# Optimization experiments

Measured on AMD Instinct MI355X. Metric: run time of the kernel, lower is better.

The kernel has to match this reference:

```python
import jax, jax.numpy as jnp
import numpy as np

N_NODES = 100000
N_EDGES = 3200000
F_IN, HIDDEN, N_CLASSES = 512, 256, 40


def setup_inputs() -> dict:
    key = jax.random.key(0)
    ks = jax.random.split(key, 8)
    x = jax.random.normal(ks[0], (N_NODES, F_IN), dtype=jnp.float32)
    edge_row = jax.random.randint(ks[1], (N_EDGES,), 0, N_NODES, dtype=jnp.int64)
    edge_col = jax.random.randint(ks[2], (N_EDGES,), 0, N_NODES, dtype=jnp.int64)
    edge_val = jax.random.uniform(ks[3], (N_EDGES,), dtype=jnp.float32)
    # Xavier-uniform-ish weights
    lim1 = float(np.sqrt(6.0 / (F_IN + HIDDEN)))
    lim2 = float(np.sqrt(6.0 / (HIDDEN + N_CLASSES)))
    W1 = jax.random.uniform(ks[4], (F_IN, HIDDEN), minval=-lim1, maxval=lim1, dtype=jnp.float32)
    b1 = jnp.zeros((HIDDEN,), dtype=jnp.float32)
    W2 = jax.random.uniform(ks[5], (HIDDEN, N_CLASSES), minval=-lim2, maxval=lim2, dtype=jnp.float32)
    b2 = jnp.zeros((N_CLASSES,), dtype=jnp.float32)
    return {"x": x, "edge_row": edge_row, "edge_col": edge_col, "edge_val": edge_val,
            "W1": W1, "b1": b1, "W2": W2, "b2": b2}


def _spmm(edge_row, edge_col, edge_val, h):
    # out[r] = sum_e val[e] * h[col[e]] for edges with row[e]==r  (a @ h)
    msg = edge_val[:, None] * h[edge_col]            # [E, F] gather + scale
    return jax.ops.segment_sum(msg, edge_row, num_segments=N_NODES)


def reference(x, edge_row, edge_col, edge_val, W1, b1, W2, b2):
    # Layer 1: dense mm -> spmm -> bias -> relu (dropout in eval mode = identity)
    h = _spmm(edge_row, edge_col, edge_val, x @ W1) + b1
    h = jax.nn.relu(h)
    # Layer 2: dense mm -> spmm -> bias
    logits = _spmm(edge_row, edge_col, edge_val, h @ W2) + b2
    return jax.nn.log_softmax(logits, axis=1)
```

## Files before the change

kernel.cpp:

```cpp
#include <hip/hip_runtime.h>
#include <math.h>

#define NN  100000
#define NE  3200000
#define FIN 512
#define HID 256
#define NC  40

#define NBUK 391
#define SPB  9472
#define BIN_BLOCKS 512
#define CHUNK ((NE + BIN_BLOCKS - 1) / BIN_BLOCKS)
#define COLMASK 0x1FFFF

typedef __attribute__((ext_vector_type(8))) short short8;
typedef __attribute__((ext_vector_type(4))) float f32x4;

__device__ inline float bf2f(unsigned short u) {
    unsigned int x = ((unsigned int)u) << 16;
    return __builtin_bit_cast(float, x);
}
__device__ inline unsigned short f2bfu(float f) {
    unsigned int x = __builtin_bit_cast(unsigned int, f);
    unsigned int r = (x + 0x7fffu + ((x >> 16) & 1u)) >> 16;
    return (unsigned short)r;
}
__device__ inline signed char q8(float v, float s) {
    int q = (int)rintf(v * s);
    q = max(-127, min(127, q));
    return (signed char)q;
}
__device__ inline unsigned cvtpk_bf16(float lo, float hi) {
    unsigned r;
    asm("v_cvt_pk_bf16_f32 %0, %1, %2" : "=v"(r) : "v"(lo), "v"(hi));
    return r;
}

__global__ __launch_bounds__(256) void k_bin(const int* __restrict__ er, const int* __restrict__ ec,
                                             const float* __restrict__ ev, int* __restrict__ bcnt,
                                             int2* __restrict__ spack) {
    __shared__ int hist[NBUK];
    __shared__ int base[NBUK];
    __shared__ int lcur[NBUK];
    for (int i = threadIdx.x; i < NBUK; i += 256) { hist[i] = 0; lcur[i] = 0; }
    __syncthreads();
    int start = blockIdx.x * CHUNK;
    int end = min(start + CHUNK, NE);
    for (int e = start + threadIdx.x; e < end; e += 256)
        atomicAdd(&hist[er[e] >> 8], 1);
    __syncthreads();
    for (int i = threadIdx.x; i < NBUK; i += 256) {
        int h = hist[i];
        base[i] = h ? atomicAdd(&bcnt[i], h) : 0;
    }
    __syncthreads();
    for (int e = start + threadIdx.x; e < end; e += 256) {
        int r = er[e];
        int b = r >> 8;
        int ofs = atomicAdd(&lcur[b], 1);
        int2 p;
        p.x = ((r & 255) << 17) | ec[e];
        p.y = __builtin_bit_cast(int, ev[e]);
        spack[(size_t)b * SPB + base[b] + ofs] = p;
    }
}

__global__ __launch_bounds__(256) void k_finecsr(const int2* __restrict__ spack, const int* __restrict__ bcnt,
                                                 int2* __restrict__ cpack,
                                                 int* __restrict__ row_beg, int* __restrict__ row_cnt) {
    __shared__ int cnt[256];
    __shared__ int sm[256];
    __shared__ int cur[256];
    int tid = threadIdx.x;
    int buk = blockIdx.x;
    size_t bb = (size_t)buk * SPB;
    int n = min(bcnt[buk], SPB);
    cnt[tid] = 0;
    __syncthreads();
    for (int i = tid; i < n; i += 256) {
        int lr = ((unsigned)spack[bb + i].x) >> 17;
        atomicAdd(&cnt[lr], 1);
    }
    __syncthreads();
    int v = cnt[tid];
    sm[tid] = v;
    __syncthreads();
    for (int off = 1; off < 256; off <<= 1) {
        int t = (tid >= off) ? sm[tid - off] : 0;
        __syncthreads();
        sm[tid] += t;
        __syncthreads();
    }
    int ex = sm[tid] - v;
    cur[tid] = ex;
    int grow = buk * 256 + tid;
    if (grow < NN) {
        row_beg[grow] = (int)bb + ex;
        row_cnt[grow] = v;
    }
    __syncthreads();
    for (int i = tid; i < n; i += 256) {
        int2 p = spack[bb + i];
        int lr = ((unsigned)p.x) >> 17;
        int pos = atomicAdd(&cur[lr], 1);
        int2 q;
        q.x = p.x & COLMASK;
        q.y = p.y;
        cpack[bb + pos] = q;
    }
}

__global__ __launch_bounds__(256) void k_w1t(const float* __restrict__ W1, unsigned short* __restrict__ W1T) {
    int b = blockIdx.x;
    int n = threadIdx.x;
    unsigned short tmp[16];
#pragma unroll
    for (int kk = 0; kk < 16; kk++)
        tmp[kk] = f2bfu(W1[(size_t)(b * 16 + kk) * HID + n]);
    unsigned short* dst = W1T + (size_t)n * FIN + b * 16;
    *(short8*)dst = *(short8*)tmp;
    *(short8*)(dst + 8) = *(short8*)(tmp + 8);
}

__global__ __launch_bounds__(256) void k_w2t(const float* __restrict__ W2, unsigned short* __restrict__ W2T) {
    int n = blockIdx.x;
    int k = threadIdx.x;
    float v = (n < NC) ? W2[(size_t)k * NC + n] : 0.f;
    W2T[(size_t)n * HID + k] = f2bfu(v);
}

__global__ __launch_bounds__(256) void k_gemm1(const float* __restrict__ x, const unsigned short* __restrict__ W1T,
                                               signed char* __restrict__ h1) {
    __shared__ unsigned short As[2][128][40];
    __shared__ unsigned short Bs[2][128][40];
    const int tid = threadIdx.x;
    const int row0 = (blockIdx.x >> 1) * 128;
    const int col0 = (blockIdx.x & 1) * 128;
    const int lane = tid & 63;
    const int w = tid >> 6;
    const int wr = (w >> 1) * 64;
    const int wc = (w & 1) * 64;
    const int m16 = lane & 15;
    const int quad = lane >> 4;

    const int srow = tid >> 1;
    const int skoff = (tid & 1) * 16;
    int gar = row0 + srow;
    if (gar >= NN) gar = NN - 1;
    const float* ax = x + (size_t)gar * FIN + skoff;
    const unsigned short* bw = W1T + (size_t)(col0 + srow) * FIN + skoff;

    f32x4 acc[4][4];
#pragma unroll
    for (int i = 0; i < 4; i++)
#pragma unroll
        for (int j = 0; j < 4; j++) acc[i][j] = (f32x4){0.f, 0.f, 0.f, 0.f};

    float4 va[4];
    uint4 vb0, vb1;

#define G1_LOAD(tt)                                                        \
    {                                                                      \
        const float* ap = ax + (tt) * 32;                                  \
        va[0] = *(const float4*)(ap);                                      \
        va[1] = *(const float4*)(ap + 4);                                  \
        va[2] = *(const float4*)(ap + 8);                                  \
        va[3] = *(const float4*)(ap + 12);                                 \
        const unsigned short* bp = bw + (tt) * 32;                         \
        vb0 = *(const uint4*)(bp);                                         \
        vb1 = *(const uint4*)(bp + 8);                                     \
    }

#define G1_STORE(bf)                                                       \
    {                                                                      \
        uint4 pa0, pa1;                                                    \
        pa0.x = cvtpk_bf16(va[0].x, va[0].y);                              \
        pa0.y = cvtpk_bf16(va[0].z, va[0].w);                              \
        pa0.z = cvtpk_bf16(va[1].x, va[1].y);                              \
        pa0.w = cvtpk_bf16(va[1].z, va[1].w);                              \
        pa1.x = cvtpk_bf16(va[2].x, va[2].y);                              \
        pa1.y = cvtpk_bf16(va[2].z, va[2].w);                              \
        pa1.z = cvtpk_bf16(va[3].x, va[3].y);                              \
        pa1.w = cvtpk_bf16(va[3].z, va[3].w);                              \
        *(uint4*)(&As[bf][srow][skoff]) = pa0;                             \
        *(uint4*)(&As[bf][srow][skoff + 8]) = pa1;                         \
        *(uint4*)(&Bs[bf][srow][skoff]) = vb0;                             \
        *(uint4*)(&Bs[bf][srow][skoff + 8]) = vb1;                         \
    }

    G1_LOAD(0)
    G1_STORE(0)
    G1_LOAD(1)
    __syncthreads();

    for (int t = 0; t < 16; ++t) {
        const int buf = t & 1;
        short8 af[4], bfr[4];
#pragma unroll
        for (int i = 0; i < 4; i++) af[i] = *(const short8*)(&As[buf][wr + i * 16 + m16][quad * 8]);
#pragma unroll
        for (int j = 0; j < 4; j++) bfr[j] = *(const short8*)(&Bs[buf][wc + j * 16 + m16][quad * 8]);
        if (t < 15) {
            G1_STORE(buf ^ 1)
            if (t < 14) G1_LOAD(t + 2)
        }
#pragma unroll
        for (int i = 0; i < 4; i++)
#pragma unroll
            for (int j = 0; j < 4; j++)
                acc[i][j] = __builtin_amdgcn_mfma_f32_16x16x32_bf16(af[i], bfr[j], acc[i][j], 0, 0, 0);
        __syncthreads();
    }
#undef G1_LOAD
#undef G1_STORE

#pragma unroll
    for (int i = 0; i < 4; i++) {
#pragma unroll
        for (int r = 0; r < 4; r++) {
            int gr = row0 + wr + i * 16 + quad * 4 + r;
            if (gr < NN) {
#pragma unroll
                for (int j = 0; j < 4; j++) {
                    int c = col0 + wc + j * 16 + m16;
                    h1[(size_t)gr * HID + c] = q8(acc[i][j][r], 16.f);
                }
            }
        }
    }
}

__global__ __launch_bounds__(256) void k_spmm1(const signed char* __restrict__ h1,
                                               const int2* __restrict__ cpack,
                                               const int* __restrict__ row_beg, const int* __restrict__ row_cnt,
                                               const float* __restrict__ b1, unsigned short* __restrict__ a1) {
    const int lane = threadIdx.x & 63;
    const int q = lane >> 4;
    const int t = lane & 15;
    const int row = ((int)(blockIdx.x * 256 + threadIdx.x) >> 6) * 4 + q;
    if (row >= NN) return;
    const int beg = row_beg[row];
    const int end = beg + row_cnt[row];
    float s[16];
#pragma unroll
    for (int i = 0; i < 16; i++) s[i] = 0.f;
    const signed char* hp = h1 + t * 16;
    int e = beg;
    for (; e + 8 <= end; e += 8) {
        unsigned long long m[8];
#pragma unroll
        for (int j = 0; j < 8; j++)
            m[j] = __builtin_nontemporal_load((const unsigned long long*)(cpack + e + j));
        int4 g[8];
#pragma unroll
        for (int j = 0; j < 8; j++) {
            unsigned c = (unsigned)m[j];
            g[j] = *(const int4*)(hp + (size_t)(c << 8));
        }
#pragma unroll
        for (int j = 0; j < 8; j++) {
            const float v = __builtin_bit_cast(float, (unsigned)(m[j] >> 32)) * 0.0625f;
#pragma unroll
            for (int d = 0; d < 4; d++) {
                const int r = ((const int*)&g[j])[d];
                s[d * 4 + 0] = fmaf(v, (float)((r << 24) >> 24), s[d * 4 + 0]);
                s[d * 4 + 1] = fmaf(v, (float)((r << 16) >> 24), s[d * 4 + 1]);
                s[d * 4 + 2] = fmaf(v, (float)((r << 8) >> 24), s[d * 4 + 2]);
                s[d * 4 + 3] = fmaf(v, (float)(r >> 24), s[d * 4 + 3]);
            }
        }
    }
    for (; e < end; e++) {
        int2 mm = cpack[e];
        const float v = __builtin_bit_cast(float, mm.y) * 0.0625f;
        int4 gg = *(const int4*)(hp + ((size_t)(unsigned)mm.x << 8));
#pragma unroll
        for (int d = 0; d < 4; d++) {
            const int r = ((const int*)&gg)[d];
            s[d * 4 + 0] = fmaf(v, (float)((r << 24) >> 24), s[d * 4 + 0]);
            s[d * 4 + 1] = fmaf(v, (float)((r << 16) >> 24), s[d * 4 + 1]);
            s[d * 4 + 2] = fmaf(v, (float)((r << 8) >> 24), s[d * 4 + 2]);
            s[d * 4 + 3] = fmaf(v, (float)(r >> 24), s[d * 4 + 3]);
        }
    }
    const int col = t * 16;
    unsigned short o[16];
#pragma unroll
    for (int d = 0; d < 4; d++) {
        const float4 bb = *(const float4*)(b1 + col + d * 4);
        o[d * 4 + 0] = f2bfu(fmaxf(s[d * 4 + 0] + bb.x, 0.f));
        o[d * 4 + 1] = f2bfu(fmaxf(s[d * 4 + 1] + bb.y, 0.f));
        o[d * 4 + 2] = f2bfu(fmaxf(s[d * 4 + 2] + bb.z, 0.f));
        o[d * 4 + 3] = f2bfu(fmaxf(s[d * 4 + 3] + bb.w, 0.f));
    }
    unsigned short* op = a1 + (size_t)row * HID + col;
    *(short8*)op = *(short8*)o;
    *(short8*)(op + 8) = *(short8*)(o + 8);
}

__global__ __launch_bounds__(256) void k_gemm2(const unsigned short* __restrict__ a1,
                                               const unsigned short* __restrict__ W2T, signed char* __restrict__ h2) {
    const int tid = threadIdx.x;
    const int lane = tid & 63;
    const int w = tid >> 6;
    const int m16 = lane & 15;
    const int quad = lane >> 4;
    const int r0 = blockIdx.x * 256 + w * 64;

    f32x4 acc[4][3];
#pragma unroll
    for (int i = 0; i < 4; i++)
#pragma unroll
        for (int j = 0; j < 3; j++) acc[i][j] = (f32x4){0.f, 0.f, 0.f, 0.f};

    for (int k0 = 0; k0 < HID; k0 += 32) {
        short8 af[4], bfr[3];
#pragma unroll
        for (int i = 0; i < 4; i++) {
            int gr = r0 + i * 16 + m16;
            if (gr >= NN) gr = NN - 1;
            af[i] = *(const short8*)(a1 + (size_t)gr * HID + k0 + quad * 8);
        }
#pragma unroll
        for (int j = 0; j < 3; j++)
            bfr[j] = *(const short8*)(W2T + (size_t)(j * 16 + m16) * HID + k0 + quad * 8);
#pragma unroll
        for (int i = 0; i < 4; i++)
#pragma unroll
            for (int j = 0; j < 3; j++)
                acc[i][j] = __builtin_amdgcn_mfma_f32_16x16x32_bf16(af[i], bfr[j], acc[i][j], 0, 0, 0);
    }
#pragma unroll
    for (int i = 0; i < 4; i++) {
#pragma unroll
        for (int r = 0; r < 4; r++) {
            int gr = r0 + i * 16 + quad * 4 + r;
            if (gr < NN) {
#pragma unroll
                for (int j = 0; j < 3; j++) {
                    int c = j * 16 + m16;
                    if (c < NC) h2[(size_t)gr * 64 + c] = q8(acc[i][j][r], 4.f);
                }
            }
        }
    }
}

__global__ __launch_bounds__(256) void k_spmm2(const signed char* __restrict__ h2,
                                               const int2* __restrict__ cpack,
                                               const int* __restrict__ row_beg, const int* __restrict__ row_cnt,
                                               const float* __restrict__ b2, float* __restrict__ out) {
    const int lane = threadIdx.x & 63;
    const int q = lane >> 4;
    const int t = lane & 15;
    const int row = ((int)(blockIdx.x * 256 + threadIdx.x) >> 6) * 4 + q;
    if (row >= NN) return;
    const bool act = t < 10;
    const int off = t * 4;
    const int boff = act ? off : 0;
    const int beg = row_beg[row];
    const int end = beg + row_cnt[row];
    float a[4] = {0.f, 0.f, 0.f, 0.f};
    const signed char* hp = h2 + off;
    int e = beg;
    for (; e + 8 <= end; e += 8) {
        unsigned long long m[8];
#pragma unroll
        for (int j = 0; j < 8; j++)
            m[j] = __builtin_nontemporal_load((const unsigned long long*)(cpack + e + j));
        int g[8];
#pragma unroll
        for (int j = 0; j < 8; j++) {
            unsigned c = (unsigned)m[j];
            g[j] = *(const int*)(hp + (size_t)(c << 6));
        }
#pragma unroll
        for (int j = 0; j < 8; j++) {
            const float v = __builtin_bit_cast(float, (unsigned)(m[j] >> 32)) * 0.25f;
            const int r = g[j];
            a[0] = fmaf(v, (float)((r << 24) >> 24), a[0]);
            a[1] = fmaf(v, (float)((r << 16) >> 24), a[1]);
            a[2] = fmaf(v, (float)((r << 8) >> 24), a[2]);
            a[3] = fmaf(v, (float)(r >> 24), a[3]);
        }
    }
    for (; e < end; e++) {
        int2 mm = cpack[e];
        const float v = __builtin_bit_cast(float, mm.y) * 0.25f;
        const int r = *(const int*)(hp + ((size_t)(unsigned)mm.x << 6));
        a[0] = fmaf(v, (float)((r << 24) >> 24), a[0]);
        a[1] = fmaf(v, (float)((r << 16) >> 24), a[1]);
        a[2] = fmaf(v, (float)((r << 8) >> 24), a[2]);
        a[3] = fmaf(v, (float)(r >> 24), a[3]);
    }
    const float4 bb = *(const float4*)(b2 + boff);
    float acc[4];
    acc[0] = a[0] + bb.x; acc[1] = a[1] + bb.y; acc[2] = a[2] + bb.z; acc[3] = a[3] + bb.w;
    float mx = act ? fmaxf(fmaxf(acc[0], acc[1]), fmaxf(acc[2], acc[3])) : -INFINITY;
#pragma unroll
    for (int o = 1; o < 16; o <<= 1) mx = fmaxf(mx, __shfl_xor(mx, o, 16));
    float se = 0.f;
    if (act) {
#pragma unroll
        for (int i = 0; i < 4; i++) se += expf(acc[i] - mx);
    }
#pragma unroll
    for (int o = 1; o < 16; o <<= 1) se += __shfl_xor(se, o, 16);
    const float ls = logf(se);
    if (act) {
        float4 r;
        r.x = acc[0] - mx - ls;
        r.y = acc[1] - mx - ls;
        r.z = acc[2] - mx - ls;
        r.w = acc[3] - mx - ls;
        *(float4*)(out + (size_t)row * NC + off) = r;
    }
}

extern "C" void kernel_launch(void* const* d_in, const int* in_sizes, int n_in, void* d_out, int out_size,
                              void* d_ws, size_t ws_size, hipStream_t stream) {
    const float* x  = (const float*)d_in[0];
    const int*   er = (const int*)d_in[1];
    const int*   ec = (const int*)d_in[2];
    const float* ev = (const float*)d_in[3];
    const float* W1 = (const float*)d_in[4];
    const float* b1 = (const float*)d_in[5];
    const float* W2 = (const float*)d_in[6];
    const float* b2 = (const float*)d_in[7];
    float* out = (float*)d_out;
    char* ws = (char*)d_ws;

    int2*  spack       = (int2*)(ws + 0);
    signed char* h1    = (signed char*)(ws + 0);
    unsigned short* a1 = (unsigned short*)(ws + 29628416);
    signed char* h2    = (signed char*)(ws + 80828416);
    int2*  cpack       = (int2*)(ws + 87228416);
    int*   row_beg     = (int*)(ws + 116856832);
    int*   row_cnt     = (int*)(ws + 117256832);
    int*   bcnt        = (int*)(ws + 117656832);
    unsigned short* W1T = (unsigned short*)(ws + 117658880);
    unsigned short* W2T = (unsigned short*)(ws + 117921024);

    hipMemsetAsync(bcnt, 0, NBUK * sizeof(int), stream);
    k_w1t<<<32, 256, 0, stream>>>(W1, W1T);
    k_w2t<<<48, 256, 0, stream>>>(W2, W2T);
    k_bin<<<BIN_BLOCKS, 256, 0, stream>>>(er, ec, ev, bcnt, spack);
    k_finecsr<<<NBUK, 256, 0, stream>>>(spack, bcnt, cpack, row_beg, row_cnt);
    k_gemm1<<<1564, 256, 0, stream>>>(x, W1T, h1);
    k_spmm1<<<(NN + 15) / 16, 256, 0, stream>>>(h1, cpack, row_beg, row_cnt, b1, a1);
    k_gemm2<<<(NN + 255) / 256, 256, 0, stream>>>(a1, W2T, h2);
    k_spmm2<<<(NN + 15) / 16, 256, 0, stream>>>(h2, cpack, row_beg, row_cnt, b2, out);
}
```

Before: 654.8 us.

## Assign one wavefront per row in SpMM, store int8 as offset-binary with ubyte converts

Both SpMM kernels now map a full 64-lane wavefront to each output row instead of 16 lanes. In layer 1 each lane gathers 4 bytes per edge, and in layer 2 four edge slots are processed in parallel and reduced with cross-lane shuffles. Quantized activations are stored as unsigned bytes offset by 128, so v_cvt_f32_ubyteN can unpack them, and the offset is removed with one correction term using the summed edge weights. The goal is more memory parallelism per row and cheaper unpacking. The costs are four times as many waves, padded loads clamped to the last edge, and lower occupancy per row in layer 1.

```diff
diff --git a/kernel.cpp b/kernel.cpp
--- a/kernel.cpp
+++ b/kernel.cpp
@@ -35,6 +35,10 @@
     asm("v_cvt_pk_bf16_f32 %0, %1, %2" : "=v"(r) : "v"(lo), "v"(hi));
     return r;
 }
+__device__ inline float cub0(int r) { float f; asm("v_cvt_f32_ubyte0 %0, %1" : "=v"(f) : "v"(r)); return f; }
+__device__ inline float cub1(int r) { float f; asm("v_cvt_f32_ubyte1 %0, %1" : "=v"(f) : "v"(r)); return f; }
+__device__ inline float cub2(int r) { float f; asm("v_cvt_f32_ubyte2 %0, %1" : "=v"(f) : "v"(r)); return f; }
+__device__ inline float cub3(int r) { float f; asm("v_cvt_f32_ubyte3 %0, %1" : "=v"(f) : "v"(r)); return f; }
 
 __global__ __launch_bounds__(256) void k_bin(const int* __restrict__ er, const int* __restrict__ ec,
                                              const float* __restrict__ ev, int* __restrict__ bcnt,
@@ -130,7 +134,7 @@
 }
 
 __global__ __launch_bounds__(256) void k_gemm1(const float* __restrict__ x, const unsigned short* __restrict__ W1T,
-                                               signed char* __restrict__ h1) {
+                                               unsigned char* __restrict__ h1) {
     __shared__ unsigned short As[2][128][40];
     __shared__ unsigned short Bs[2][128][40];
     const int tid = threadIdx.x;
@@ -223,83 +227,64 @@
 #pragma unroll
                 for (int j = 0; j < 4; j++) {
                     int c = col0 + wc + j * 16 + m16;
-                    h1[(size_t)gr * HID + c] = q8(acc[i][j][r], 16.f);
+                    h1[(size_t)gr * HID + c] = (unsigned char)(q8(acc[i][j][r], 16.f) + 128);
                 }
             }
         }
     }
 }
 
-__global__ __launch_bounds__(256) void k_spmm1(const signed char* __restrict__ h1,
+__global__ __launch_bounds__(256) void k_spmm1(const unsigned char* __restrict__ h1,
                                                const int2* __restrict__ cpack,
                                                const int* __restrict__ row_beg, const int* __restrict__ row_cnt,
                                                const float* __restrict__ b1, unsigned short* __restrict__ a1) {
     const int lane = threadIdx.x & 63;
-    const int q = lane >> 4;
-    const int t = lane & 15;
-    const int row = ((int)(blockIdx.x * 256 + threadIdx.x) >> 6) * 4 + q;
+    const int row = (int)__builtin_amdgcn_readfirstlane(blockIdx.x * 4 + (threadIdx.x >> 6));
     if (row >= NN) return;
-    const int beg = row_beg[row];
-    const int end = beg + row_cnt[row];
-    float s[16];
-#pragma unroll
-    for (int i = 0; i < 16; i++) s[i] = 0.f;
-    const signed char* hp = h1 + t * 16;
-    int e = beg;
-    for (; e + 8 <= end; e += 8) {
-        unsigned long long m[8];
-#pragma unroll
-        for (int j = 0; j < 8; j++)
-            m[j] = __builtin_nontemporal_load((const unsigned long long*)(cpack + e + j));
-        int4 g[8];
-#pragma unroll
-        for (int j = 0; j < 8; j++) {
-            unsigned c = (unsigned)m[j];
-            g[j] = *(const int4*)(hp + (size_t)(c << 8));
-        }
-#pragma unroll
-        for (int j = 0; j < 8; j++) {
-            const float v = __builtin_bit_cast(float, (unsigned)(m[j] >> 32)) * 0.0625f;
-#pragma unroll
-            for (int d = 0; d < 4; d++) {
-                const int r = ((const int*)&g[j])[d];
-                s[d * 4 + 0] = fmaf(v, (float)((r << 24) >> 24), s[d * 4 + 0]);
-                s[d * 4 + 1] = fmaf(v, (float)((r << 16) >> 24), s[d * 4 + 1]);
-                s[d * 4 + 2] = fmaf(v, (float)((r << 8) >> 24), s[d * 4 + 2]);
-                s[d * 4 + 3] = fmaf(v, (float)(r >> 24), s[d * 4 + 3]);
-            }
-        }
-    }
-    for (; e < end; e++) {
-        int2 mm = cpack[e];
-        const float v = __builtin_bit_cast(float, mm.y) * 0.0625f;
-        int4 gg = *(const int4*)(hp + ((size_t)(unsigned)mm.x << 8));
-#pragma unroll
-        for (int d = 0; d < 4; d++) {
-            const int r = ((const int*)&gg)[d];
-            s[d * 4 + 0] = fmaf(v, (float)((r << 24) >> 24), s[d * 4 + 0]);
-            s[d * 4 + 1] = fmaf(v, (float)((r << 16) >> 24), s[d * 4 + 1]);
-            s[d * 4 + 2] = fmaf(v, (float)((r << 8) >> 24), s[d * 4 + 2]);
-            s[d * 4 + 3] = fmaf(v, (float)(r >> 24), s[d * 4 + 3]);
-        }
-    }
-    const int col = t * 16;
-    unsigned short o[16];
-#pragma unroll
-    for (int d = 0; d < 4; d++) {
-        const float4 bb = *(const float4*)(b1 + col + d * 4);
-        o[d * 4 + 0] = f2bfu(fmaxf(s[d * 4 + 0] + bb.x, 0.f));
-        o[d * 4 + 1] = f2bfu(fmaxf(s[d * 4 + 1] + bb.y, 0.f));
-        o[d * 4 + 2] = f2bfu(fmaxf(s[d * 4 + 2] + bb.z, 0.f));
-        o[d * 4 + 3] = f2bfu(fmaxf(s[d * 4 + 3] + bb.w, 0.f));
-    }
-    unsigned short* op = a1 + (size_t)row * HID + col;
-    *(short8*)op = *(short8*)o;
-    *(short8*)(op + 8) = *(short8*)(o + 8);
+    const int beg = (int)__builtin_amdgcn_readfirstlane(row_beg[row]);
+    const int cnt = (int)__builtin_amdgcn_readfirstlane(row_cnt[row]);
+    const int end = beg + cnt;
+    const int voff = lane * 4;
+    float su[4] = {0.f, 0.f, 0.f, 0.f};
+    float sv = 0.f;
+
+    for (int e0 = beg; e0 < end; e0 += 16) {
+        unsigned cb[16];
+        float vv[16];
+#pragma unroll
+        for (int j = 0; j < 16; j++) {
+            int idx = e0 + j;
+            int cl = idx < end ? idx : end - 1;
+            int2 p = cpack[cl];
+            cb[j] = ((unsigned)p.x & COLMASK) << 8;
+            vv[j] = idx < end ? __builtin_bit_cast(float, p.y) * 0.0625f : 0.f;
+        }
+        int g[16];
+#pragma unroll
+        for (int j = 0; j < 16; j++)
+            g[j] = *(const int*)(h1 + (size_t)cb[j] + voff);
+#pragma unroll
+        for (int j = 0; j < 16; j++) {
+            sv += vv[j];
+            su[0] = fmaf(vv[j], cub0(g[j]), su[0]);
+            su[1] = fmaf(vv[j], cub1(g[j]), su[1]);
+            su[2] = fmaf(vv[j], cub2(g[j]), su[2]);
+            su[3] = fmaf(vv[j], cub3(g[j]), su[3]);
+        }
+    }
+
+    const int col = lane * 4;
+    const float4 bb = *(const float4*)(b1 + col);
+    ushort4 o;
+    o.x = f2bfu(fmaxf(fmaf(-128.f, sv, su[0]) + bb.x, 0.f));
+    o.y = f2bfu(fmaxf(fmaf(-128.f, sv, su[1]) + bb.y, 0.f));
+    o.z = f2bfu(fmaxf(fmaf(-128.f, sv, su[2]) + bb.z, 0.f));
+    o.w = f2bfu(fmaxf(fmaf(-128.f, sv, su[3]) + bb.w, 0.f));
+    *(ushort4*)(a1 + (size_t)row * HID + col) = o;
 }
 
 __global__ __launch_bounds__(256) void k_gemm2(const unsigned short* __restrict__ a1,
-                                               const unsigned short* __restrict__ W2T, signed char* __restrict__ h2) {
+                                               const unsigned short* __restrict__ W2T, unsigned char* __restrict__ h2) {
     const int tid = threadIdx.x;
     const int lane = tid & 63;
     const int w = tid >> 6;
@@ -339,63 +324,71 @@
 #pragma unroll
                 for (int j = 0; j < 3; j++) {
                     int c = j * 16 + m16;
-                    if (c < NC) h2[(size_t)gr * 64 + c] = q8(acc[i][j][r], 4.f);
+                    if (c < NC) h2[(size_t)gr * 64 + c] = (unsigned char)(q8(acc[i][j][r], 4.f) + 128);
                 }
             }
         }
     }
 }
 
-__global__ __launch_bounds__(256) void k_spmm2(const signed char* __restrict__ h2,
+__global__ __launch_bounds__(256) void k_spmm2(const unsigned char* __restrict__ h2,
                                                const int2* __restrict__ cpack,
                                                const int* __restrict__ row_beg, const int* __restrict__ row_cnt,
                                                const float* __restrict__ b2, float* __restrict__ out) {
     const int lane = threadIdx.x & 63;
-    const int q = lane >> 4;
+    const int slot = lane >> 4;
     const int t = lane & 15;
-    const int row = ((int)(blockIdx.x * 256 + threadIdx.x) >> 6) * 4 + q;
+    const int row = (int)__builtin_amdgcn_readfirstlane(blockIdx.x * 4 + (threadIdx.x >> 6));
     if (row >= NN) return;
+    const int beg = (int)__builtin_amdgcn_readfirstlane(row_beg[row]);
+    const int cnt = (int)__builtin_amdgcn_readfirstlane(row_cnt[row]);
+    const int end = beg + cnt;
+    const int t4 = t * 4;
+    float su[4] = {0.f, 0.f, 0.f, 0.f};
+    float sv = 0.f;
+
+    for (int e0 = beg; e0 < end; e0 += 16) {
+        unsigned cb[4];
+        float vs[4];
+#pragma unroll
+        for (int u = 0; u < 4; u++) {
+            int idx = e0 + u * 4 + slot;
+            int cl = idx < end ? idx : end - 1;
+            int2 p = cpack[cl];
+            cb[u] = ((unsigned)p.x & COLMASK) << 6;
+            vs[u] = idx < end ? __builtin_bit_cast(float, p.y) * 0.25f : 0.f;
+        }
+        int g[4];
+#pragma unroll
+        for (int u = 0; u < 4; u++)
+            g[u] = *(const int*)(h2 + (size_t)cb[u] + t4);
+#pragma unroll
+        for (int u = 0; u < 4; u++) {
+            sv += vs[u];
+            su[0] = fmaf(vs[u], cub0(g[u]), su[0]);
+            su[1] = fmaf(vs[u], cub1(g[u]), su[1]);
+            su[2] = fmaf(vs[u], cub2(g[u]), su[2]);
+            su[3] = fmaf(vs[u], cub3(g[u]), su[3]);
+        }
+    }
+
+#pragma unroll
+    for (int i = 0; i < 4; i++) {
+        su[i] += __shfl_xor(su[i], 16, 64);
+        su[i] += __shfl_xor(su[i], 32, 64);
+    }
+    sv += __shfl_xor(sv, 16, 64);
+    sv += __shfl_xor(sv, 32, 64);
+
     const bool act = t < 10;
-    const int off = t * 4;
+    const int off = t4;
     const int boff = act ? off : 0;
-    const int beg = row_beg[row];
-    const int end = beg + row_cnt[row];
-    float a[4] = {0.f, 0.f, 0.f, 0.f};
-    const signed char* hp = h2 + off;
-    int e = beg;
-    for (; e + 8 <= end; e += 8) {
-        unsigned long long m[8];
-#pragma unroll
-        for (int j = 0; j < 8; j++)
-            m[j] = __builtin_nontemporal_load((const unsigned long long*)(cpack + e + j));
-        int g[8];
-#pragma unroll
-        for (int j = 0; j < 8; j++) {
-            unsigned c = (unsigned)m[j];
-            g[j] = *(const int*)(hp + (size_t)(c << 6));
-        }
-#pragma unroll
-        for (int j = 0; j < 8; j++) {
-            const float v = __builtin_bit_cast(float, (unsigned)(m[j] >> 32)) * 0.25f;
-            const int r = g[j];
-            a[0] = fmaf(v, (float)((r << 24) >> 24), a[0]);
-            a[1] = fmaf(v, (float)((r << 16) >> 24), a[1]);
-            a[2] = fmaf(v, (float)((r << 8) >> 24), a[2]);
-            a[3] = fmaf(v, (float)(r >> 24), a[3]);
-        }
-    }
-    for (; e < end; e++) {
-        int2 mm = cpack[e];
-        const float v = __builtin_bit_cast(float, mm.y) * 0.25f;
-        const int r = *(const int*)(hp + ((size_t)(unsigned)mm.x << 6));
-        a[0] = fmaf(v, (float)((r << 24) >> 24), a[0]);
-        a[1] = fmaf(v, (float)((r << 16) >> 24), a[1]);
-        a[2] = fmaf(v, (float)((r << 8) >> 24), a[2]);
-        a[3] = fmaf(v, (float)(r >> 24), a[3]);
-    }
     const float4 bb = *(const float4*)(b2 + boff);
     float acc[4];
-    acc[0] = a[0] + bb.x; acc[1] = a[1] + bb.y; acc[2] = a[2] + bb.z; acc[3] = a[3] + bb.w;
+    acc[0] = fmaf(-128.f, sv, su[0]) + bb.x;
+    acc[1] = fmaf(-128.f, sv, su[1]) + bb.y;
+    acc[2] = fmaf(-128.f, sv, su[2]) + bb.z;
+    acc[3] = fmaf(-128.f, sv, su[3]) + bb.w;
     float mx = act ? fmaxf(fmaxf(acc[0], acc[1]), fmaxf(acc[2], acc[3])) : -INFINITY;
 #pragma unroll
     for (int o = 1; o < 16; o <<= 1) mx = fmaxf(mx, __shfl_xor(mx, o, 16));
@@ -407,7 +400,7 @@
 #pragma unroll
     for (int o = 1; o < 16; o <<= 1) se += __shfl_xor(se, o, 16);
     const float ls = logf(se);
-    if (act) {
+    if (act && slot == 0) {
         float4 r;
         r.x = acc[0] - mx - ls;
         r.y = acc[1] - mx - ls;
@@ -431,9 +424,9 @@
     char* ws = (char*)d_ws;
 
     int2*  spack       = (int2*)(ws + 0);
-    signed char* h1    = (signed char*)(ws + 0);
+    unsigned char* h1  = (unsigned char*)(ws + 0);
     unsigned short* a1 = (unsigned short*)(ws + 29628416);
-    signed char* h2    = (signed char*)(ws + 80828416);
+    unsigned char* h2  = (unsigned char*)(ws + 80828416);
     int2*  cpack       = (int2*)(ws + 87228416);
     int*   row_beg     = (int*)(ws + 116856832);
     int*   row_cnt     = (int*)(ws + 117256832);
@@ -447,7 +440,7 @@
     k_bin<<<BIN_BLOCKS, 256, 0, stream>>>(er, ec, ev, bcnt, spack);
     k_finecsr<<<NBUK, 256, 0, stream>>>(spack, bcnt, cpack, row_beg, row_cnt);
     k_gemm1<<<1564, 256, 0, stream>>>(x, W1T, h1);
-    k_spmm1<<<(NN + 15) / 16, 256, 0, stream>>>(h1, cpack, row_beg, row_cnt, b1, a1);
+    k_spmm1<<<NN / 4, 256, 0, stream>>>(h1, cpack, row_beg, row_cnt, b1, a1);
     k_gemm2<<<(NN + 255) / 256, 256, 0, stream>>>(a1, W2T, h2);
-    k_spmm2<<<(NN + 15) / 16, 256, 0, stream>>>(h2, cpack, row_beg, row_cnt, b2, out);
-}
+    k_spmm2<<<NN / 4, 256, 0, stream>>>(h2, cpack, row_beg, row_cnt, b2, out);
+}
```

After: 640.5 us. 1.02x faster.
